# Performance work log

Measured on AMD Instinct MI355X. Metric: run time of the kernel, lower is better.

Reference implementation:

```python
import jax, jax.numpy as jnp
import numpy as np

D_MODEL = 512
NHEAD = 8
D_HEAD = D_MODEL // NHEAD
SCALE = D_HEAD ** -0.5
EPS = 1e-8


def setup_inputs() -> dict:
    key = jax.random.key(0)
    ks = jax.random.split(key, 12)
    B, N = 4, 2048
    s = D_MODEL ** -0.5
    return {
        "Q_input": jax.random.normal(ks[0], (B, N, D_MODEL), jnp.float32),
        "KV_input": jax.random.normal(ks[1], (B, N, D_MODEL), jnp.float32),
        "SC": jax.random.uniform(ks[2], (B, N, N), jnp.float32),
        "Wq_w": jax.random.normal(ks[3], (D_MODEL, D_MODEL), jnp.float32) * s,
        "Wq_b": jnp.zeros((D_MODEL,), jnp.float32),
        "Wk_w": jax.random.normal(ks[4], (D_MODEL, D_MODEL), jnp.float32) * s,
        "Wk_b": jnp.zeros((D_MODEL,), jnp.float32),
        "Wv_w": jax.random.normal(ks[5], (D_MODEL, D_MODEL), jnp.float32) * s,
        "Wv_b": jnp.zeros((D_MODEL,), jnp.float32),
        "gate_w": jax.random.normal(ks[6], (), jnp.float32),
        "gate_b": jnp.zeros((), jnp.float32),
        "out_w": jax.random.normal(ks[7], (D_MODEL, D_MODEL), jnp.float32) * s,
        "out_b": jnp.zeros((D_MODEL,), jnp.float32),
    }


def reference(Q_input, KV_input, SC, Wq_w, Wq_b, Wk_w, Wk_b, Wv_w, Wv_b,
              gate_w, gate_b, out_w, out_b):
    B, N, _ = Q_input.shape
    # projections -> [B, H, N, d_head]
    def proj(x, w, b):
        y = x @ w.T + b
        return y.reshape(B, N, NHEAD, D_HEAD).transpose(0, 2, 1, 3)
    Q = proj(Q_input, Wq_w, Wq_b)
    K = proj(KV_input, Wk_w, Wk_b)
    V = proj(KV_input, Wv_w, Wv_b)
    # scores [B, H, N, N]
    scores = jnp.einsum('bhqd,bhkd->bhqk', Q, K) * SCALE
    # per-edge gate: sigmoid(w*SC + b), broadcast over heads
    g = jax.nn.sigmoid(SC * gate_w + gate_b)  # [B, N, N]
    scores = scores + jnp.log(g + EPS)[:, None, :, :]
    attn = jax.nn.softmax(scores, axis=-1)
    out = jnp.einsum('bhqk,bhkd->bhqd', attn, V)
    out = out.transpose(0, 2, 1, 3).reshape(B, N, D_MODEL)
    return out @ out_w.T + out_b
```

## Files before the change

### kernel.cpp

```cpp
#include <hip/hip_runtime.h>

typedef unsigned short u16;
typedef unsigned int u32;
typedef __attribute__((ext_vector_type(4))) float f32x4;
typedef __attribute__((ext_vector_type(8))) short s16x8;
typedef __attribute__((ext_vector_type(4))) u16 u16x4;

#define L2E 1.4426950408889634f
#define QSCALE 0.18033688011112042f

__device__ __forceinline__ float bf2f(u16 u) {
    union { u32 i; float f; } v; v.i = ((u32)u) << 16; return v.f;
}
__device__ __forceinline__ u16 f2bf(float f) {
    union { float f; u32 i; } v; v.f = f;
    return (u16)((v.i + 0x7fffu + ((v.i >> 16) & 1u)) >> 16);
}
__device__ __forceinline__ u32 pack_hi(float a, float b) {
    union { float f; u32 i; } x, y; x.f = a; y.f = b;
    return (x.i >> 16) | (y.i & 0xFFFF0000u);
}

__device__ __forceinline__ void gl2lds16(const u16* g, u16* l) {
    __builtin_amdgcn_global_load_lds(
        (const __attribute__((address_space(1))) void*)g,
        (__attribute__((address_space(3))) void*)l, 16, 0, 0);
}

__global__ __launch_bounds__(256) void prep_kernel(
    const float* __restrict__ s0, const float* __restrict__ s1,
    const float* __restrict__ s2, const float* __restrict__ s3,
    const float* __restrict__ s4, const float* __restrict__ s5,
    u16* __restrict__ dst,
    const float* __restrict__ SC, const float* __restrict__ gwp,
    const float* __restrict__ gbp, u16* __restrict__ LGx)
{
    if (blockIdx.x < 9216) {
        int e = (blockIdx.x * 256 + threadIdx.x) * 4;
        const float* src; int off;
        if      (e < 4194304) { src = s0; off = e; }
        else if (e < 8388608) { src = s1; off = e - 4194304; }
        else if (e < 8650752) { src = s2; off = e - 8388608; }
        else if (e < 8912896) { src = s3; off = e - 8650752; }
        else if (e < 9175040) { src = s4; off = e - 8912896; }
        else                  { src = s5; off = e - 9175040; }
        f32x4 f = *(const f32x4*)(src + off);
        u16x4 o;
#pragma unroll
        for (int j = 0; j < 4; ++j) o[j] = f2bf(f[j]);
        *(u16x4*)(dst + e) = o;
    } else {
        const int flat = (blockIdx.x - 9216) * 256 + threadIdx.x;
        const int lane = flat & 63;
        const int kt   = (flat >> 6) & 31;
        const int t16  = (flat >> 11) & 127;
        const int b    = flat >> 18;
        const int l16 = lane & 15, quad = lane >> 4;
        const float tA = -gwp[0] * L2E, tB = -gbp[0] * L2E;
        const float* row = SC + ((size_t)b * 2048 + t16 * 16 + l16) * 2048
                              + kt * 64 + quad * 4;
        __align__(16) u16 tmp[16];
#pragma unroll
        for (int kk = 0; kk < 4; ++kk) {
            f32x4 x = *(const f32x4*)(row + kk * 16);
#pragma unroll
            for (int reg = 0; reg < 4; ++reg) {
                float g = __builtin_amdgcn_rcpf(
                    1.0f + __builtin_amdgcn_exp2f(tA * x[reg] + tB)) + 1e-8f;
                tmp[kk * 4 + reg] = f2bf(__builtin_amdgcn_logf(g));
            }
        }
        u16* d = LGx + (size_t)flat * 16;
        *(uint4*)d       = *(uint4*)tmp;
        *(uint4*)(d + 8) = *(uint4*)(tmp + 8);
    }
}

__device__ __forceinline__ void gemm_core(
    const u16* __restrict__ A, const u16* __restrict__ Bw,
    int m0, int n0, u16* As, u16* Bs, f32x4 acc[4][4])
{
    const int tid = threadIdx.x;
    const int lane = tid & 63, w = tid >> 6;
    const int wm = w >> 1, wn = w & 1;
    const int l16 = lane & 15, quad = lane >> 4;
    const int srow = (lane >> 2), sch = (lane & 3) * 8;
    const f32x4 vzero = {0.f, 0.f, 0.f, 0.f};
#pragma unroll
    for (int i = 0; i < 4; ++i)
#pragma unroll
        for (int j = 0; j < 4; ++j) acc[i][j] = vzero;

#pragma unroll
    for (int j = 0; j < 2; ++j) {
        int row = w * 32 + j * 16 + srow;
        gl2lds16(&A[(size_t)(m0 + row) * 512 + sch], &As[w * 1024 + j * 512]);
        gl2lds16(&Bw[(size_t)(n0 + row) * 512 + sch], &Bs[w * 1024 + j * 512]);
    }
    for (int kt = 0; kt < 16; ++kt) {
        __syncthreads();
        const int cur = (kt & 1) * 4096;
        if (kt < 15) {
            const int nxt = ((kt + 1) & 1) * 4096;
#pragma unroll
            for (int j = 0; j < 2; ++j) {
                int row = w * 32 + j * 16 + srow;
                gl2lds16(&A[(size_t)(m0 + row) * 512 + (kt + 1) * 32 + sch],
                         &As[nxt + w * 1024 + j * 512]);
                gl2lds16(&Bw[(size_t)(n0 + row) * 512 + (kt + 1) * 32 + sch],
                         &Bs[nxt + w * 1024 + j * 512]);
            }
        }
        s16x8 af[4], bfr[4];
#pragma unroll
        for (int mt = 0; mt < 4; ++mt)
            af[mt] = *(const s16x8*)&As[cur + (wm * 64 + mt * 16 + l16) * 32 + quad * 8];
#pragma unroll
        for (int nt = 0; nt < 4; ++nt)
            bfr[nt] = *(const s16x8*)&Bs[cur + (wn * 64 + nt * 16 + l16) * 32 + quad * 8];
#pragma unroll
        for (int mt = 0; mt < 4; ++mt)
#pragma unroll
            for (int nt = 0; nt < 4; ++nt)
                acc[mt][nt] = __builtin_amdgcn_mfma_f32_16x16x32_bf16(
                    af[mt], bfr[nt], acc[mt][nt], 0, 0, 0);
    }
}

__global__ __launch_bounds__(256) void proj_kernel(
    const u16* __restrict__ cQin, const u16* __restrict__ cKV,
    const u16* __restrict__ cW,
    const float* __restrict__ bq, const float* __restrict__ bk,
    const float* __restrict__ bv,
    u16* __restrict__ Qh, u16* __restrict__ Kh, u16* __restrict__ Vt)
{
    __shared__ __align__(16) u16 As[2 * 4096];
    __shared__ __align__(16) u16 Bs[2 * 4096];
    const int job = blockIdx.z;
    const u16* A = (job == 0) ? cQin : cKV;
    const u16* W = cW + (size_t)job * 262144;
    const float* bias = (job == 0) ? bq : (job == 1 ? bk : bv);
    const int m0 = blockIdx.y * 128, n0 = blockIdx.x * 128;
    f32x4 acc[4][4];
    gemm_core(A, W, m0, n0, As, Bs, acc);

    const int tid = threadIdx.x, lane = tid & 63, w = tid >> 6;
    const int wm = w >> 1, wn = w & 1, l16 = lane & 15, quad = lane >> 4;
#pragma unroll
    for (int nt = 0; nt < 4; ++nt) {
        int j = n0 + wn * 64 + nt * 16 + l16;
        float bj = bias[j];
        int h = j >> 6, d = j & 63;
#pragma unroll
        for (int mt = 0; mt < 4; ++mt) {
            int trow = m0 + wm * 64 + mt * 16 + quad * 4;
            int bb = trow >> 11, nn = trow & 2047;
            int bh = bb * 8 + h;
            if (job == 2) {
                u16x4 pv;
#pragma unroll
                for (int reg = 0; reg < 4; ++reg) pv[reg] = f2bf(acc[mt][nt][reg] + bj);
                *(u16x4*)&Vt[(size_t)(bh * 64 + d) * 2048 + nn] = pv;
            } else if (job == 0) {
#pragma unroll
                for (int reg = 0; reg < 4; ++reg)
                    Qh[(size_t)(bh * 2048 + nn + reg) * 64 + d] =
                        f2bf((acc[mt][nt][reg] + bj) * QSCALE);
            } else {
#pragma unroll
                for (int reg = 0; reg < 4; ++reg)
                    Kh[(size_t)(bh * 2048 + nn + reg) * 64 + d] =
                        f2bf(acc[mt][nt][reg] + bj);
            }
        }
    }
}

__global__ __launch_bounds__(512, 4) void attn_kernel(
    const u16* __restrict__ Qh, const u16* __restrict__ Kh,
    const u16* __restrict__ Vt, const u16* __restrict__ LGx,
    u16* __restrict__ Ob)
{
    __shared__ __align__(16) u16 Ks[2][4096];
    __shared__ __align__(16) u16 Vs[2][4096];
    __shared__ __align__(16) u16 Plds[8][16][68];
    const int tid = threadIdx.x;
    const int w = tid >> 6, lane = tid & 63;
    const int l16 = lane & 15, quad = lane >> 4;
    const int b = blockIdx.z, head = blockIdx.y, qg = blockIdx.x;
    const int bh = b * 8 + head;
    const int q0 = qg * 128 + w * 16;
    const int t16 = qg * 8 + w;
    const u16* Qp = Qh + (size_t)bh * 131072;
    const u16* Kp = Kh + (size_t)bh * 131072;
    const u16* Vp = Vt + (size_t)bh * 131072;
    const u16* LGt = LGx + ((size_t)((b * 128 + t16) * 32) * 64 + lane) * 16;
    const f32x4 vzero = {0.f, 0.f, 0.f, 0.f};
    const s16x8 ones = {0x3F80, 0x3F80, 0x3F80, 0x3F80,
                        0x3F80, 0x3F80, 0x3F80, 0x3F80};

    const int sr = lane >> 3;
    const int scw = ((lane & 7) ^ sr) * 8;
    const int slab = (w & 3) * 16;
    const bool isK = (w < 4);
    const u16* sG0 = isK ? (Kp + (size_t)(slab + sr) * 64 + scw)
                         : (Vp + (size_t)(slab + sr) * 2048 + scw);
    const u16* sG1 = isK ? (Kp + (size_t)(slab + 8 + sr) * 64 + scw)
                         : (Vp + (size_t)(slab + 8 + sr) * 2048 + scw);
    const size_t sAdv = isK ? 4096 : 64;
    u16* sL0 = isK ? &Ks[0][slab * 64] : &Vs[0][slab * 64];
    u16* sL1 = isK ? &Ks[0][(slab + 8) * 64] : &Vs[0][(slab + 8) * 64];

    s16x8 qf[2];
#pragma unroll
    for (int kc = 0; kc < 2; ++kc)
        qf[kc] = *(const s16x8*)&Qp[(size_t)(q0 + l16) * 64 + kc * 32 + quad * 8];
    f32x4 o[4], lacc = vzero;
#pragma unroll
    for (int dn = 0; dn < 4; ++dn) o[dn] = vzero;

    gl2lds16(sG0, sL0);
    gl2lds16(sG1, sL1);

    for (int kt = 0; kt < 32; ++kt) {
        __syncthreads();
        const int cur = kt & 1;
        if (kt < 31) {
            const int nxt = cur ^ 1;
            gl2lds16(sG0 + (size_t)(kt + 1) * sAdv, sL0 + nxt * 4096);
            gl2lds16(sG1 + (size_t)(kt + 1) * sAdv, sL1 + nxt * 4096);
        }
        const u16* Kb = &Ks[cur][0];
        const u16* Vb = &Vs[cur][0];
        __align__(16) u16 lgv[16];
        *(uint4*)lgv       = *(const uint4*)(LGt + (size_t)kt * 1024);
        *(uint4*)(lgv + 8) = *(const uint4*)(LGt + (size_t)kt * 1024 + 8);

        f32x4 st[4];
#pragma unroll
        for (int kc = 0; kc < 2; ++kc) {
            s16x8 kf[4];
#pragma unroll
            for (int kk = 0; kk < 4; ++kk)
                kf[kk] = *(const s16x8*)&Kb[(kk * 16 + l16) * 64 +
                                            ((kc * 4 + quad) ^ (l16 & 7)) * 8];
#pragma unroll
            for (int kk = 0; kk < 4; ++kk)
                st[kk] = __builtin_amdgcn_mfma_f32_16x16x32_bf16(
                    kf[kk], qf[kc], kc == 0 ? vzero : st[kk], 0, 0, 0);
        }
#pragma unroll
        for (int kk = 0; kk < 4; ++kk) {
            float p0 = __builtin_amdgcn_exp2f(st[kk][0] + bf2f(lgv[kk * 4 + 0]));
            float p1 = __builtin_amdgcn_exp2f(st[kk][1] + bf2f(lgv[kk * 4 + 1]));
            float p2 = __builtin_amdgcn_exp2f(st[kk][2] + bf2f(lgv[kk * 4 + 2]));
            float p3 = __builtin_amdgcn_exp2f(st[kk][3] + bf2f(lgv[kk * 4 + 3]));
            uint2 pk = {pack_hi(p0, p1), pack_hi(p2, p3)};
            *(uint2*)&Plds[w][l16][kk * 16 + quad * 4] = pk;
        }
#pragma unroll
        for (int kc = 0; kc < 2; ++kc) {
            s16x8 pf = *(const s16x8*)&Plds[w][l16][kc * 32 + quad * 8];
            lacc = __builtin_amdgcn_mfma_f32_16x16x32_bf16(pf, ones, lacc, 0, 0, 0);
            s16x8 vf[4];
#pragma unroll
            for (int dn = 0; dn < 4; ++dn)
                vf[dn] = *(const s16x8*)&Vb[(dn * 16 + l16) * 64 +
                                            ((kc * 4 + quad) ^ (l16 & 7)) * 8];
#pragma unroll
            for (int dn = 0; dn < 4; ++dn)
                o[dn] = __builtin_amdgcn_mfma_f32_16x16x32_bf16(
                    pf, vf[dn], o[dn], 0, 0, 0);
        }
    }
#pragma unroll
    for (int reg = 0; reg < 4; ++reg) {
        float inv = __builtin_amdgcn_rcpf(lacc[reg]);
        int trow = b * 2048 + q0 + quad * 4 + reg;
#pragma unroll
        for (int dn = 0; dn < 4; ++dn)
            Ob[(size_t)trow * 512 + head * 64 + dn * 16 + l16] =
                f2bf(o[dn][reg] * inv);
    }
}

__global__ __launch_bounds__(256) void out_kernel(
    const u16* __restrict__ Ob, const u16* __restrict__ cWo,
    const float* __restrict__ bo, float* __restrict__ out)
{
    __shared__ __align__(16) u16 As[2 * 4096];
    __shared__ __align__(16) u16 Bs[2 * 4096];
    const int m0 = blockIdx.y * 128, n0 = blockIdx.x * 128;
    f32x4 acc[4][4];
    gemm_core(Ob, cWo, m0, n0, As, Bs, acc);
    const int tid = threadIdx.x, lane = tid & 63, w = tid >> 6;
    const int wm = w >> 1, wn = w & 1, l16 = lane & 15, quad = lane >> 4;
#pragma unroll
    for (int nt = 0; nt < 4; ++nt) {
        int j = n0 + wn * 64 + nt * 16 + l16;
        float bj = bo[j];
#pragma unroll
        for (int mt = 0; mt < 4; ++mt) {
            int t = m0 + wm * 64 + mt * 16 + quad * 4;
#pragma unroll
            for (int reg = 0; reg < 4; ++reg)
                out[(size_t)(t + reg) * 512 + j] = acc[mt][nt][reg] + bj;
        }
    }
}

extern "C" void kernel_launch(void* const* d_in, const int* in_sizes, int n_in,
                              void* d_out, int out_size, void* d_ws, size_t ws_size,
                              hipStream_t stream)
{
    const float* Qin  = (const float*)d_in[0];
    const float* KVin = (const float*)d_in[1];
    const float* SC   = (const float*)d_in[2];
    const float* Wq   = (const float*)d_in[3];
    const float* bq   = (const float*)d_in[4];
    const float* Wk   = (const float*)d_in[5];
    const float* bk   = (const float*)d_in[6];
    const float* Wv   = (const float*)d_in[7];
    const float* bv   = (const float*)d_in[8];
    const float* gw   = (const float*)d_in[9];
    const float* gb   = (const float*)d_in[10];
    const float* Wo   = (const float*)d_in[11];
    const float* bo   = (const float*)d_in[12];
    float* out = (float*)d_out;

    u16* conv = (u16*)d_ws;
    u16* cQin = conv;
    u16* cKV  = conv + 4194304;
    u16* cW   = conv + 8388608;
    u16* Qh   = conv + 9437184;
    u16* Kh   = Qh + 4194304;
    u16* Vt   = Kh + 4194304;
    u16* Ob   = Vt + 4194304;
    u16* LGx  = Ob + 4194304;

    hipLaunchKernelGGL(prep_kernel, dim3(13312), dim3(256), 0, stream,
                       Qin, KVin, Wq, Wk, Wv, Wo, conv, SC, gw, gb, LGx);
    hipLaunchKernelGGL(proj_kernel, dim3(4, 64, 3), dim3(256), 0, stream,
                       cQin, cKV, cW, bq, bk, bv, Qh, Kh, Vt);
    hipLaunchKernelGGL(attn_kernel, dim3(16, 8, 4), dim3(512), 0, stream,
                       Qh, Kh, Vt, LGx, Ob);
    hipLaunchKernelGGL(out_kernel, dim3(4, 64), dim3(256), 0, stream,
                       Ob, cW + 786432, bo, out);
}
```

Measured before the change: 246.1 us.

## Replace P LDS round-trip with permlane swaps, fold log-gate into MFMA accumulator

The attention kernel no longer writes the bf16 probability tile to shared memory and reads it back. Instead it rearranges the packed P values across lanes with permlane32/permlane16 swap intrinsics into the MFMA A-operand layout. The log-gate bias is now loaded one tile ahead into registers and used as the initial MFMA accumulator, which removes the separate per-element adds. This saves LDS traffic and LDS space and hides gate-load latency, at the cost of more registers and a dependence on the exact lane permutation being correct.

```diff
diff --git a/kernel.cpp b/kernel.cpp
--- a/kernel.cpp
+++ b/kernel.cpp
@@ -5,6 +5,7 @@
 typedef __attribute__((ext_vector_type(4))) float f32x4;
 typedef __attribute__((ext_vector_type(8))) short s16x8;
 typedef __attribute__((ext_vector_type(4))) u16 u16x4;
+typedef __attribute__((ext_vector_type(2))) u32 u32x2;
 
 #define L2E 1.4426950408889634f
 #define QSCALE 0.18033688011112042f
@@ -19,6 +20,12 @@
 __device__ __forceinline__ u32 pack_hi(float a, float b) {
     union { float f; u32 i; } x, y; x.f = a; y.f = b;
     return (x.i >> 16) | (y.i & 0xFFFF0000u);
+}
+__device__ __forceinline__ float bflo(u32 w) {
+    union { u32 i; float f; } v; v.i = w << 16; return v.f;
+}
+__device__ __forceinline__ float bfhi(u32 w) {
+    union { u32 i; float f; } v; v.i = w & 0xFFFF0000u; return v.f;
 }
 
 __device__ __forceinline__ void gl2lds16(const u16* g, u16* l) {
@@ -183,7 +190,6 @@
 {
     __shared__ __align__(16) u16 Ks[2][4096];
     __shared__ __align__(16) u16 Vs[2][4096];
-    __shared__ __align__(16) u16 Plds[8][16][68];
     const int tid = threadIdx.x;
     const int w = tid >> 6, lane = tid & 63;
     const int l16 = lane & 15, quad = lane >> 4;
@@ -222,6 +228,9 @@
     gl2lds16(sG0, sL0);
     gl2lds16(sG1, sL1);
 
+    uint4 lgA = *(const uint4*)LGt;
+    uint4 lgB = *(const uint4*)(LGt + 8);
+
     for (int kt = 0; kt < 32; ++kt) {
         __syncthreads();
         const int cur = kt & 1;
@@ -232,9 +241,23 @@
         }
         const u16* Kb = &Ks[cur][0];
         const u16* Vb = &Vs[cur][0];
-        __align__(16) u16 lgv[16];
-        *(uint4*)lgv       = *(const uint4*)(LGt + (size_t)kt * 1024);
-        *(uint4*)(lgv + 8) = *(const uint4*)(LGt + (size_t)kt * 1024 + 8);
+
+        f32x4 cin[4];
+        {
+            const u32 wd[8] = {lgA.x, lgA.y, lgA.z, lgA.w,
+                               lgB.x, lgB.y, lgB.z, lgB.w};
+#pragma unroll
+            for (int kk = 0; kk < 4; ++kk) {
+                cin[kk][0] = bflo(wd[kk * 2]);
+                cin[kk][1] = bfhi(wd[kk * 2]);
+                cin[kk][2] = bflo(wd[kk * 2 + 1]);
+                cin[kk][3] = bfhi(wd[kk * 2 + 1]);
+            }
+        }
+        if (kt < 31) {
+            lgA = *(const uint4*)(LGt + (size_t)(kt + 1) * 1024);
+            lgB = *(const uint4*)(LGt + (size_t)(kt + 1) * 1024 + 8);
+        }
 
         f32x4 st[4];
 #pragma unroll
@@ -247,20 +270,33 @@
 #pragma unroll
             for (int kk = 0; kk < 4; ++kk)
                 st[kk] = __builtin_amdgcn_mfma_f32_16x16x32_bf16(
-                    kf[kk], qf[kc], kc == 0 ? vzero : st[kk], 0, 0, 0);
-        }
+                    kf[kk], qf[kc], kc == 0 ? cin[kk] : st[kk], 0, 0, 0);
+        }
+
+        u32 Pw[4][2];
 #pragma unroll
         for (int kk = 0; kk < 4; ++kk) {
-            float p0 = __builtin_amdgcn_exp2f(st[kk][0] + bf2f(lgv[kk * 4 + 0]));
-            float p1 = __builtin_amdgcn_exp2f(st[kk][1] + bf2f(lgv[kk * 4 + 1]));
-            float p2 = __builtin_amdgcn_exp2f(st[kk][2] + bf2f(lgv[kk * 4 + 2]));
-            float p3 = __builtin_amdgcn_exp2f(st[kk][3] + bf2f(lgv[kk * 4 + 3]));
-            uint2 pk = {pack_hi(p0, p1), pack_hi(p2, p3)};
-            *(uint2*)&Plds[w][l16][kk * 16 + quad * 4] = pk;
-        }
+            float p0 = __builtin_amdgcn_exp2f(st[kk][0]);
+            float p1 = __builtin_amdgcn_exp2f(st[kk][1]);
+            float p2 = __builtin_amdgcn_exp2f(st[kk][2]);
+            float p3 = __builtin_amdgcn_exp2f(st[kk][3]);
+            Pw[kk][0] = pack_hi(p0, p1);
+            Pw[kk][1] = pack_hi(p2, p3);
+        }
+
 #pragma unroll
         for (int kc = 0; kc < 2; ++kc) {
-            s16x8 pf = *(const s16x8*)&Plds[w][l16][kc * 32 + quad * 8];
+            union { u32 wrd[4]; s16x8 v; } pu;
+#pragma unroll
+            for (int i = 0; i < 2; ++i) {
+                u32x2 r1 = __builtin_amdgcn_permlane32_swap(
+                    Pw[2 * kc][i], Pw[2 * kc + 1][i], false, false);
+                u32x2 r2 = __builtin_amdgcn_permlane16_swap(
+                    r1[0], r1[1], false, false);
+                pu.wrd[i]     = r2[0];
+                pu.wrd[2 + i] = r2[1];
+            }
+            s16x8 pf = pu.v;
             lacc = __builtin_amdgcn_mfma_f32_16x16x32_bf16(pf, ones, lacc, 0, 0, 0);
             s16x8 vf[4];
 #pragma unroll
```

New measurement: 240.9 us. 1.02x faster.
